# Kernel tuning notes

Hardware: AMD Instinct MI355X
Metric: run time of the kernel (lower is better)

The kernel has to match this reference:

```python
import jax, jax.numpy as jnp
import numpy as np

N_CHEM = 200000
N_GENE = 20000
N_EDGES = 1000000
IN, HID, OUT = 128, 256, 128


def _seg_mean(msg, dst, num_segments):
    # DGL fn.mean: mean of incoming messages; nodes with zero in-degree get 0.
    s = jax.ops.segment_sum(msg, dst, num_segments=num_segments)
    cnt = jax.ops.segment_sum(jnp.ones((msg.shape[0],), msg.dtype), dst,
                              num_segments=num_segments)[:, None]
    return jnp.where(cnt > 0, s / jnp.maximum(cnt, 1.0), 0.0)


def setup_inputs() -> dict:
    key = jax.random.key(0)
    ks = jax.random.split(key, 12)
    d = {
        'src_cg': jax.random.randint(ks[0], (N_EDGES,), 0, N_CHEM, dtype=jnp.int32),
        'dst_cg': jax.random.randint(ks[1], (N_EDGES,), 0, N_GENE, dtype=jnp.int32),
        'src_gc': jax.random.randint(ks[2], (N_EDGES,), 0, N_GENE, dtype=jnp.int32),
        'dst_gc': jax.random.randint(ks[3], (N_EDGES,), 0, N_CHEM, dtype=jnp.int32),
        'embed_chem': jax.random.normal(ks[4], (N_CHEM, IN), jnp.float32) * 0.1,
        'embed_gene': jax.random.normal(ks[5], (N_GENE, IN), jnp.float32) * 0.1,
        'W1_cg': jax.random.normal(ks[6], (IN, HID), jnp.float32) * (1.0 / np.sqrt(IN)),
        'b1_cg': jnp.zeros((HID,), jnp.float32),
        'W1_gc': jax.random.normal(ks[7], (IN, HID), jnp.float32) * (1.0 / np.sqrt(IN)),
        'b1_gc': jnp.zeros((HID,), jnp.float32),
        'W2_cg': jax.random.normal(ks[8], (HID, OUT), jnp.float32) * (1.0 / np.sqrt(HID)),
        'b2_cg': jnp.zeros((OUT,), jnp.float32),
        'W2_gc': jax.random.normal(ks[9], (HID, OUT), jnp.float32) * (1.0 / np.sqrt(HID)),
        'b2_gc': jnp.zeros((OUT,), jnp.float32),
    }
    return d


def _layer(h_chem, h_gene, W_cg, b_cg, W_gc, b_gc, src_cg, dst_cg, src_gc, dst_gc):
    # per-etype linear transform on source features
    Wh_cg = h_chem @ W_cg + b_cg   # [N_CHEM, D]
    Wh_gc = h_gene @ W_gc + b_gc   # [N_GENE, D]
    # copy_u + mean per etype; multi_update_all('sum') -> single etype per dst here
    new_gene = _seg_mean(Wh_cg[src_cg], dst_cg, N_GENE)
    new_chem = _seg_mean(Wh_gc[src_gc], dst_gc, N_CHEM)
    return new_chem, new_gene


def reference(src_cg, dst_cg, src_gc, dst_gc, embed_chem, embed_gene,
              W1_cg, b1_cg, W1_gc, b1_gc, W2_cg, b2_cg, W2_gc, b2_gc):
    h_chem, h_gene = _layer(embed_chem, embed_gene, W1_cg, b1_cg, W1_gc, b1_gc,
                            src_cg, dst_cg, src_gc, dst_gc)
    h_chem = jax.nn.leaky_relu(h_chem, negative_slope=0.01)
    h_gene = jax.nn.leaky_relu(h_gene, negative_slope=0.01)
    h_chem, _ = _layer(h_chem, h_gene, W2_cg, b2_cg, W2_gc, b2_gc,
                       src_cg, dst_cg, src_gc, dst_gc)
    return h_chem  # [N_CHEM, OUT]
```

## Files before the change

kernel.cpp:

```cpp
#include <hip/hip_runtime.h>
#include <stdint.h>
#include <stddef.h>

#define N_CHEM 200000
#define N_GENE 20000
#define N_EDGES 1000000
#define IN_D 128
#define HID_D 256
#define OUT_D 128
#define N_SEG (N_GENE + N_CHEM)

#define NGB 313
#define NCB 391
#define NB  (NGB + NCB)
#define EPB 2048
#define NBA ((2 * N_EDGES + EPB - 1) / EPB)
#define CAP 8192
#define DROPPED 0x80000000

typedef float nfloat4 __attribute__((ext_vector_type(4)));
typedef __attribute__((ext_vector_type(8))) short bf16x8;
typedef __attribute__((ext_vector_type(4))) float f32x4;

__device__ inline unsigned bf16rne(float x) {
    unsigned u = __float_as_uint(x);
    return (u + 0x7FFFu + ((u >> 16) & 1u)) >> 16;
}

__device__ inline int bucket_of(int slot) {
    return (slot < N_GENE) ? (slot >> 6) : (NGB + ((slot - N_GENE) >> 9));
}
__device__ inline int bucket_slot0(int b) {
    return (b < NGB) ? (b << 6) : (N_GENE + ((b - NGB) << 9));
}


__global__ __launch_bounds__(256) void place_convert_kernel(
        const int* __restrict__ src_cg, const int* __restrict__ dst_cg,
        const int* __restrict__ src_gc, const int* __restrict__ dst_gc,
        int* __restrict__ bcur, unsigned* __restrict__ records,
        const float* __restrict__ conv_in, unsigned short* __restrict__ conv_out) {
    if ((int)blockIdx.x >= NBA) {
        int cb = blockIdx.x - NBA;
        const int tid = threadIdx.x;
        #pragma unroll
        for (int q = 0; q < 4; ++q) {
            int i = cb * 1024 + q * 256 + tid;
            if (i < N_CHEM * IN_D / 4) {
                float4 v = *(const float4*)&conv_in[(size_t)i * 4];
                uint2 w;
                w.x = bf16rne(v.x) | (bf16rne(v.y) << 16);
                w.y = bf16rne(v.z) | (bf16rne(v.w) << 16);
                *(uint2*)&conv_out[(size_t)i * 4] = w;
            }
        }
        return;
    }
    __shared__ unsigned stage_rec[EPB];
    __shared__ unsigned short stage_bkt[EPB];
    __shared__ int hist[NB];
    __shared__ int cursor[NB];
    __shared__ int tsum[256];
    const int tid = threadIdx.x;
    const int e0 = blockIdx.x * EPB;
    const int cnt_blk = min(EPB, 2 * N_EDGES - e0);

    for (int i = tid; i < NB; i += 256) hist[i] = 0;
    __syncthreads();

    int slotR[EPB / 256], srcR[EPB / 256];
    #pragma unroll
    for (int q = 0; q < EPB / 256; ++q) {
        int e = e0 + q * 256 + tid;
        int slot = -1, s = 0;
        if (e < N_EDGES)            { slot = dst_cg[e];                    s = src_cg[e]; }
        else if (e < 2 * N_EDGES)   { slot = N_GENE + dst_gc[e - N_EDGES]; s = src_gc[e - N_EDGES]; }
        slotR[q] = slot; srcR[q] = s;
        if (slot >= 0) atomicAdd(&hist[bucket_of(slot)], 1);
    }
    __syncthreads();

    const int b3 = tid * 3;
    int h0 = (b3     < NB) ? hist[b3]     : 0;
    int h1 = (b3 + 1 < NB) ? hist[b3 + 1] : 0;
    int h2 = (b3 + 2 < NB) ? hist[b3 + 2] : 0;
    int ts = h0 + h1 + h2;
    tsum[tid] = ts;
    __syncthreads();
    for (int off = 1; off < 256; off <<= 1) {
        int t = (tid >= off) ? tsum[tid - off] : 0;
        __syncthreads();
        tsum[tid] += t;
        __syncthreads();
    }
    int base = tsum[tid] - ts;
    if (b3     < NB) cursor[b3]     = base;
    if (b3 + 1 < NB) cursor[b3 + 1] = base + h0;
    if (b3 + 2 < NB) cursor[b3 + 2] = base + h0 + h1;
    __syncthreads();

    #pragma unroll
    for (int q = 0; q < EPB / 256; ++q) {
        int slot = slotR[q];
        if (slot >= 0) {
            int b = bucket_of(slot);
            int p = atomicAdd(&cursor[b], 1);
            stage_rec[p] = ((unsigned)(slot - bucket_slot0(b)) << 18) | (unsigned)srcR[q];
            stage_bkt[p] = (unsigned short)b;
        }
    }
    __syncthreads();

    for (int i = tid; i < NB; i += 256) {
        int n = hist[i];
        if (n) {
            int got = atomicAdd(&bcur[i], n);
            int excl_i = cursor[i] - n;
            hist[i] = (got + n <= CAP) ? (i * CAP + got - excl_i) : (int)DROPPED;
        }
    }
    __syncthreads();

    for (int i = tid; i < cnt_blk; i += 256) {
        int d = hist[stage_bkt[i]];
        if (d != (int)DROPPED) records[i + d] = stage_rec[i];
    }
}


__global__ void bucket_scan_kernel(const int* __restrict__ bcur,
                                   int* __restrict__ bbase, int* __restrict__ indptr) {
    __shared__ int sm[1024];
    const int tid = threadIdx.x;
    int v = (tid < NB) ? min(bcur[tid], CAP) : 0;
    sm[tid] = v;
    __syncthreads();
    for (int off = 1; off < 1024; off <<= 1) {
        int t = (tid >= off) ? sm[tid - off] : 0;
        __syncthreads();
        sm[tid] += t;
        __syncthreads();
    }
    if (tid < NB) bbase[tid] = sm[tid] - v;
    if (tid == NB - 1) {
        bbase[NB] = sm[tid];
        indptr[N_SEG] = sm[tid];
    }
}


__global__ __launch_bounds__(256) void bin_b_kernel(
        const unsigned* __restrict__ records, const int* __restrict__ bbase,
        const int* __restrict__ bcur,
        int* __restrict__ indptr, int* __restrict__ esrc) {
    __shared__ int hist[512];
    __shared__ int tsum[256];
    const int tid = threadIdx.x;
    const int b = blockIdx.x;
    int slot0 = bucket_slot0(b);
    int nslots = (b < NGB) ? min(64, N_GENE - slot0) : min(512, N_SEG - slot0);
    const int rbase = bbase[b];
    const int E = min(bcur[b], CAP);
    const unsigned* rec = &records[(size_t)b * CAP];

    hist[tid] = 0; hist[tid + 256] = 0;
    __syncthreads();
    for (int i = tid; i < E; i += 256)
        atomicAdd(&hist[rec[i] >> 18], 1);
    __syncthreads();

    int h0 = hist[2 * tid], h1 = hist[2 * tid + 1];
    int ts = h0 + h1;
    tsum[tid] = ts;
    __syncthreads();
    for (int off = 1; off < 256; off <<= 1) {
        int t = (tid >= off) ? tsum[tid - off] : 0;
        __syncthreads();
        tsum[tid] += t;
        __syncthreads();
    }
    int ex = tsum[tid] - ts;
    __syncthreads();
    hist[2 * tid]     = ex;
    hist[2 * tid + 1] = ex + h0;
    if (2 * tid     < nslots) indptr[slot0 + 2 * tid]     = rbase + ex;
    if (2 * tid + 1 < nslots) indptr[slot0 + 2 * tid + 1] = rbase + ex + h0;
    __syncthreads();

    for (int i = tid; i < E; i += 256) {
        unsigned r = rec[i];
        int p = atomicAdd(&hist[r >> 18], 1);
        esrc[rbase + p] = (int)(r & 0x3FFFFu);
    }
}


__device__ inline void acc_u(float* a, uint4 v) {
    a[0] += __uint_as_float(v.x << 16); a[1] += __uint_as_float(v.x & 0xffff0000u);
    a[2] += __uint_as_float(v.y << 16); a[3] += __uint_as_float(v.y & 0xffff0000u);
    a[4] += __uint_as_float(v.z << 16); a[5] += __uint_as_float(v.z & 0xffff0000u);
    a[6] += __uint_as_float(v.w << 16); a[7] += __uint_as_float(v.w & 0xffff0000u);
}


__global__ __launch_bounds__(256) void gather_mean_bf16_split_kernel(
        const unsigned short* __restrict__ table,
        const int* __restrict__ indptr, const int* __restrict__ esrc,
        unsigned short* __restrict__ outb, int n) {
    int lane = threadIdx.x & 15;
    int half = (threadIdx.x >> 4) & 1;
    int node = blockIdx.x * 8 + (threadIdx.x >> 5);
    if (node >= n) return;
    int s = indptr[node], e = indptr[node + 1];
    int deg = e - s;
    int mid = s + ((deg + 1) >> 1);
    int j0 = half ? mid : s;
    int j1 = half ? e   : mid;
    int c = lane << 3;
    float acc[8] = {};
    int j = j0;
    for (; j + 8 <= j1; j += 8) {
        int i0 = esrc[j],     i1 = esrc[j + 1], i2 = esrc[j + 2], i3 = esrc[j + 3];
        int i4 = esrc[j + 4], i5 = esrc[j + 5], i6 = esrc[j + 6], i7 = esrc[j + 7];
        uint4 v0 = *(const uint4*)&table[(size_t)i0 * 128 + c];
        uint4 v1 = *(const uint4*)&table[(size_t)i1 * 128 + c];
        uint4 v2 = *(const uint4*)&table[(size_t)i2 * 128 + c];
        uint4 v3 = *(const uint4*)&table[(size_t)i3 * 128 + c];
        uint4 v4 = *(const uint4*)&table[(size_t)i4 * 128 + c];
        uint4 v5 = *(const uint4*)&table[(size_t)i5 * 128 + c];
        uint4 v6 = *(const uint4*)&table[(size_t)i6 * 128 + c];
        uint4 v7 = *(const uint4*)&table[(size_t)i7 * 128 + c];
        acc_u(acc, v0); acc_u(acc, v1); acc_u(acc, v2); acc_u(acc, v3);
        acc_u(acc, v4); acc_u(acc, v5); acc_u(acc, v6); acc_u(acc, v7);
    }
    for (; j + 4 <= j1; j += 4) {
        uint4 v0 = *(const uint4*)&table[(size_t)esrc[j]     * 128 + c];
        uint4 v1 = *(const uint4*)&table[(size_t)esrc[j + 1] * 128 + c];
        uint4 v2 = *(const uint4*)&table[(size_t)esrc[j + 2] * 128 + c];
        uint4 v3 = *(const uint4*)&table[(size_t)esrc[j + 3] * 128 + c];
        acc_u(acc, v0); acc_u(acc, v1); acc_u(acc, v2); acc_u(acc, v3);
    }
    for (; j < j1; ++j) {
        uint4 v = *(const uint4*)&table[(size_t)esrc[j] * 128 + c];
        acc_u(acc, v);
    }
    #pragma unroll
    for (int q = 0; q < 8; ++q) acc[q] += __shfl_xor(acc[q], 16);
    if (half == 0) {
        float inv = (deg > 0) ? 1.f / (float)deg : 0.f;
        #pragma unroll
        for (int q = 0; q < 8; ++q) acc[q] *= inv;
        uint4 w;
        w.x = bf16rne(acc[0]) | (bf16rne(acc[1]) << 16);
        w.y = bf16rne(acc[2]) | (bf16rne(acc[3]) << 16);
        w.z = bf16rne(acc[4]) | (bf16rne(acc[5]) << 16);
        w.w = bf16rne(acc[6]) | (bf16rne(acc[7]) << 16);
        *(uint4*)&outb[(size_t)node * 128 + c] = w;
    }
}


template<bool NT>
__global__ __launch_bounds__(256) void gather_mean_bf16_kernel(
        const unsigned short* __restrict__ table,
        const int* __restrict__ indptr, const int* __restrict__ esrc,
        float* __restrict__ out, int n) {
    int lane = threadIdx.x & 15;
    int node = blockIdx.x * 16 + (threadIdx.x >> 4);
    if (node >= n) return;
    int s = indptr[node], e = indptr[node + 1];
    int c = lane << 3;
    float acc[8] = {};
    int j = s;
    for (; j + 4 <= e; j += 4) {
        uint4 v0 = *(const uint4*)&table[(size_t)esrc[j]     * 128 + c];
        uint4 v1 = *(const uint4*)&table[(size_t)esrc[j + 1] * 128 + c];
        uint4 v2 = *(const uint4*)&table[(size_t)esrc[j + 2] * 128 + c];
        uint4 v3 = *(const uint4*)&table[(size_t)esrc[j + 3] * 128 + c];
        acc_u(acc, v0); acc_u(acc, v1); acc_u(acc, v2); acc_u(acc, v3);
    }
    for (; j < e; ++j) {
        uint4 v = *(const uint4*)&table[(size_t)esrc[j] * 128 + c];
        acc_u(acc, v);
    }
    int deg = e - s;
    float inv = (deg > 0) ? 1.f / (float)deg : 0.f;
    #pragma unroll
    for (int q = 0; q < 8; ++q) acc[q] *= inv;
    float* dst = &out[(size_t)node * 128 + c];
    if (NT) {
        nfloat4 a = { acc[0], acc[1], acc[2], acc[3] };
        nfloat4 b = { acc[4], acc[5], acc[6], acc[7] };
        __builtin_nontemporal_store(a, (nfloat4*)dst);
        __builtin_nontemporal_store(b, (nfloat4*)(dst + 4));
    } else {
        *(float4*)dst       = make_float4(acc[0], acc[1], acc[2], acc[3]);
        *(float4*)(dst + 4) = make_float4(acc[4], acc[5], acc[6], acc[7]);
    }
}


__global__ __launch_bounds__(256) void gather_mean_f32_kernel(
        const float* __restrict__ table,
        const int* __restrict__ indptr, const int* __restrict__ esrc,
        float* __restrict__ out, int n) {
    int lane = threadIdx.x & 31;
    int node = blockIdx.x * 8 + (threadIdx.x >> 5);
    if (node >= n) return;
    int s = indptr[node], e = indptr[node + 1];
    int c = lane << 2;
    float4 acc = make_float4(0.f, 0.f, 0.f, 0.f);
    int j = s;
    for (; j + 4 <= e; j += 4) {
        int s0 = esrc[j], s1 = esrc[j + 1], s2 = esrc[j + 2], s3 = esrc[j + 3];
        float4 v0 = *(const float4*)&table[(size_t)s0 * 128 + c];
        float4 v1 = *(const float4*)&table[(size_t)s1 * 128 + c];
        float4 v2 = *(const float4*)&table[(size_t)s2 * 128 + c];
        float4 v3 = *(const float4*)&table[(size_t)s3 * 128 + c];
        acc.x += (v0.x + v1.x) + (v2.x + v3.x);
        acc.y += (v0.y + v1.y) + (v2.y + v3.y);
        acc.z += (v0.z + v1.z) + (v2.z + v3.z);
        acc.w += (v0.w + v1.w) + (v2.w + v3.w);
    }
    for (; j < e; ++j) {
        float4 v = *(const float4*)&table[(size_t)esrc[j] * 128 + c];
        acc.x += v.x; acc.y += v.y; acc.z += v.z; acc.w += v.w;
    }
    int deg = e - s;
    float inv = (deg > 0) ? 1.f / (float)deg : 0.f;
    acc.x *= inv; acc.y *= inv; acc.z *= inv; acc.w *= inv;
    *(float4*)&out[(size_t)node * 128 + c] = acc;
}


template<int K, int N, bool MASK_LEAKY>
__global__ __launch_bounds__(256) void gemm_mfma_kernel(
        const unsigned short* __restrict__ A,
        const float* __restrict__ W,
        const float* __restrict__ bias,
        const int* __restrict__ indptr,
        unsigned short* __restrict__ C,
        int M) {
    constexpr int BK  = 128;
    constexpr int LDK = BK + 8;
    __shared__ unsigned short As[64 * LDK];
    __shared__ unsigned short Ws[64 * LDK];
    const int tid  = threadIdx.x;
    const int lane = tid & 63;
    const int w    = tid >> 6;
    const int m0 = blockIdx.x * 64;
    const int n0 = blockIdx.y * 64;
    const int l15 = lane & 15;
    const int lhi = lane >> 4;
    f32x4 acc[4] = {};

    for (int kt0 = 0; kt0 < K; kt0 += BK) {
        #pragma unroll
        for (int it = 0; it < 4; ++it) {
            int idx = it * 256 + tid;
            int row = idx >> 4;
            int c8  = (idx & 15) << 3;
            uint4 v = make_uint4(0u, 0u, 0u, 0u);
            if (m0 + row < M)
                v = *(const uint4*)&A[(size_t)(m0 + row) * K + kt0 + c8];
            *(uint4*)&As[row * LDK + c8] = v;
        }
        #pragma unroll
        for (int it = 0; it < 32; ++it) {
            int i = it * 256 + tid;
            int k = i >> 6;
            int n = i & 63;
            float f = W[(size_t)(kt0 + k) * N + n0 + n];
            Ws[n * LDK + k] = (unsigned short)bf16rne(f);
        }
        __syncthreads();

        #pragma unroll
        for (int kk = 0; kk < BK; kk += 32) {
            bf16x8 a = *(const bf16x8*)&As[(w * 16 + l15) * LDK + kk + lhi * 8];
            #pragma unroll
            for (int nt = 0; nt < 4; ++nt) {
                bf16x8 b = *(const bf16x8*)&Ws[(nt * 16 + l15) * LDK + kk + lhi * 8];
                acc[nt] = __builtin_amdgcn_mfma_f32_16x16x32_bf16(a, b, acc[nt], 0, 0, 0);
            }
        }
        __syncthreads();
    }

    #pragma unroll
    for (int nt = 0; nt < 4; ++nt) {
        int col = n0 + nt * 16 + l15;
        float bz = bias[col];
        #pragma unroll
        for (int r = 0; r < 4; ++r) {
            int row = m0 + w * 16 + lhi * 4 + r;
            if (row < M) {
                float v = acc[nt][r] + bz;
                if (MASK_LEAKY) {
                    int deg = indptr[row + 1] - indptr[row];
                    v = (deg == 0) ? 0.f : (v > 0.f ? v : 0.01f * v);
                }
                C[(size_t)row * N + col] = (unsigned short)bf16rne(v);
            }
        }
    }
}


template<int K, int N, bool MASK_LEAKY, bool BF16_OUT>
__global__ __launch_bounds__(256) void gemm_kernel(const float* __restrict__ A,
                                                   const float* __restrict__ W,
                                                   const float* __restrict__ bias,
                                                   const int* __restrict__ indptr,
                                                   void* __restrict__ Cout, int M) {
    __shared__ float As[64 * 68];
    __shared__ float Ws[64 * 64];
    const int tid = threadIdx.x;
    const int tx = tid & 15, ty = tid >> 4;
    const int m0 = blockIdx.x * 64;
    const int n0 = blockIdx.y * 64;
    const int r0 = ty << 2, c0 = tx << 2;
    float acc[4][4] = {};

    for (int kt = 0; kt < K; kt += 64) {
        #pragma unroll
        for (int q = 0; q < 4; ++q) {
            int idx = tid + q * 256;
            int row = idx >> 4;
            int c4  = (idx & 15) << 2;
            float4 v = make_float4(0.f, 0.f, 0.f, 0.f);
            if (m0 + row < M)
                v = *(const float4*)&A[(size_t)(m0 + row) * K + kt + c4];
            *(float4*)&As[row * 68 + c4] = v;
        }
        #pragma unroll
        for (int q = 0; q < 4; ++q) {
            int idx = tid + q * 256;
            int k   = idx >> 4;
            int c4  = (idx & 15) << 2;
            *(float4*)&Ws[(k << 6) + c4] =
                *(const float4*)&W[(size_t)(kt + k) * N + n0 + c4];
        }
        __syncthreads();

        #pragma unroll 4
        for (int k = 0; k < 64; k += 4) {
            float a[4][4];
            #pragma unroll
            for (int r = 0; r < 4; ++r) {
                float4 v = *(const float4*)&As[(r0 + r) * 68 + k];
                a[r][0] = v.x; a[r][1] = v.y; a[r][2] = v.z; a[r][3] = v.w;
            }
            #pragma unroll
            for (int kk = 0; kk < 4; ++kk) {
                float4 w = *(const float4*)&Ws[((k + kk) << 6) + c0];
                #pragma unroll
                for (int r = 0; r < 4; ++r) {
                    acc[r][0] = fmaf(a[r][kk], w.x, acc[r][0]);
                    acc[r][1] = fmaf(a[r][kk], w.y, acc[r][1]);
                    acc[r][2] = fmaf(a[r][kk], w.z, acc[r][2]);
                    acc[r][3] = fmaf(a[r][kk], w.w, acc[r][3]);
                }
            }
        }
        __syncthreads();
    }

    float4 b = *(const float4*)&bias[n0 + c0];
    #pragma unroll
    for (int r = 0; r < 4; ++r) {
        int row = m0 + r0 + r;
        if (row < M) {
            float4 v;
            v.x = acc[r][0] + b.x; v.y = acc[r][1] + b.y;
            v.z = acc[r][2] + b.z; v.w = acc[r][3] + b.w;
            if (MASK_LEAKY) {
                int deg = indptr[row + 1] - indptr[row];
                if (deg == 0) {
                    v = make_float4(0.f, 0.f, 0.f, 0.f);
                } else {
                    v.x = v.x > 0.f ? v.x : 0.01f * v.x;
                    v.y = v.y > 0.f ? v.y : 0.01f * v.y;
                    v.z = v.z > 0.f ? v.z : 0.01f * v.z;
                    v.w = v.w > 0.f ? v.w : 0.01f * v.w;
                }
            }
            if (BF16_OUT) {
                uint2 w;
                w.x = bf16rne(v.x) | (bf16rne(v.y) << 16);
                w.y = bf16rne(v.z) | (bf16rne(v.w) << 16);
                *(uint2*)&((unsigned short*)Cout)[(size_t)row * N + n0 + c0] = w;
            } else {
                *(float4*)&((float*)Cout)[(size_t)row * N + n0 + c0] = v;
            }
        }
    }
}


extern "C" void kernel_launch(void* const* d_in, const int* in_sizes, int n_in,
                              void* d_out, int out_size, void* d_ws, size_t ws_size,
                              hipStream_t stream) {
    const int*   src_cg     = (const int*)d_in[0];
    const int*   dst_cg     = (const int*)d_in[1];
    const int*   src_gc     = (const int*)d_in[2];
    const int*   dst_gc     = (const int*)d_in[3];
    const float* embed_chem = (const float*)d_in[4];
    const float* W1_cg = (const float*)d_in[6];
    const float* b1_cg = (const float*)d_in[7];
    const float* W2_gc = (const float*)d_in[12];
    const float* b2_gc = (const float*)d_in[13];
    float* out = (float*)d_out;

    int* ws_i = (int*)d_ws;
    size_t off = 0;
    int* bcur  = ws_i + off; off += NB;
    int* bbase = ws_i + off; off += NB + 1;
    off = (off + 3) & ~(size_t)3;
    int* indptr = ws_i + off; off += N_SEG + 1; off = (off + 3) & ~(size_t)3;
    int* esrc   = ws_i + off; off += 2 * N_EDGES;
    size_t union_off = off;
    unsigned* records = (unsigned*)(ws_i + union_off);
    unsigned short* agg1b   = (unsigned short*)(ws_i + union_off);
    unsigned short* h_geneb = agg1b + (size_t)N_GENE * IN_D;
    float* agg1f   = (float*)(ws_i + union_off);
    float* h_genef = agg1f + (size_t)N_GENE * IN_D;
    size_t union_sz = (size_t)N_GENE * (IN_D + HID_D);
    off = union_off + union_sz;
    unsigned short* Wh2b = (unsigned short*)(ws_i + off); off += (size_t)N_GENE * OUT_D / 2;
    unsigned short* embedb = (unsigned short*)(ws_i + off);
    size_t off_full = off + (size_t)N_CHEM * IN_D / 2;
    const bool bf16_embed = ws_size >= off_full * sizeof(int);

    (void)hipMemsetAsync(bcur, 0, NB * sizeof(int), stream);

    const int nconv = bf16_embed ? (N_CHEM * IN_D / 4 + 1023) / 1024 : 0;
    place_convert_kernel<<<NBA + nconv, 256, 0, stream>>>(
        src_cg, dst_cg, src_gc, dst_gc, bcur, records, embed_chem, embedb);
    bucket_scan_kernel<<<1, 1024, 0, stream>>>(bcur, bbase, indptr);
    bin_b_kernel<<<NB, 256, 0, stream>>>(records, bbase, bcur, indptr, esrc);

    if (bf16_embed) {
        gather_mean_bf16_split_kernel<<<(N_GENE + 7) / 8, 256, 0, stream>>>(
            embedb, indptr, esrc, agg1b, N_GENE);
        {
            dim3 g((N_GENE + 63) / 64, HID_D / 64), blk(256);
            gemm_mfma_kernel<IN_D, HID_D, true><<<g, blk, 0, stream>>>(
                agg1b, W1_cg, b1_cg, indptr, h_geneb, N_GENE);
        }
        {
            dim3 g((N_GENE + 63) / 64, OUT_D / 64), blk(256);
            gemm_mfma_kernel<HID_D, OUT_D, false><<<g, blk, 0, stream>>>(
                h_geneb, W2_gc, b2_gc, nullptr, Wh2b, N_GENE);
        }
    } else {
        gather_mean_f32_kernel<<<(N_GENE + 7) / 8, 256, 0, stream>>>(
            embed_chem, indptr, esrc, agg1f, N_GENE);
        {
            dim3 g((N_GENE + 63) / 64, HID_D / 64), blk(256);
            gemm_kernel<IN_D, HID_D, true, false><<<g, blk, 0, stream>>>(
                agg1f, W1_cg, b1_cg, indptr, h_genef, N_GENE);
        }
        {
            dim3 g((N_GENE + 63) / 64, OUT_D / 64), blk(256);
            gemm_kernel<HID_D, OUT_D, false, true><<<g, blk, 0, stream>>>(
                h_genef, W2_gc, b2_gc, nullptr, Wh2b, N_GENE);
        }
    }

    gather_mean_bf16_kernel<true><<<(N_CHEM + 15) / 16, 256, 0, stream>>>(
        Wh2b, indptr + N_GENE, esrc, out, N_CHEM);
}
```

Baseline: 387.6 us.

## Restructure gene and chem gather kernels and enlarge edges per placement block

The gene gather no longer splits each node's edge list between two half-warps. It now splits the feature columns into four 32-column slices spread across blocks, with four lanes per node, so each block's working set of the embedding table is narrower and more cache-friendly. The chem gather now uses 8 lanes per node, each loading 16 bf16 columns, and handles 32 nodes per block to raise bytes in flight per lane. The edge-placement blocking (EPB) doubles, halving the number of placement blocks. The risks are higher register use from 16 accumulators, fewer threads per node on the gene side, and possibly worse load balance in the placement phase.

New measurement: 484.1 us. 1.25x slower.

```diff
diff --git a/kernel.cpp b/kernel.cpp
--- a/kernel.cpp
+++ b/kernel.cpp
@@ -13,7 +13,7 @@
 #define NGB 313
 #define NCB 391
 #define NB  (NGB + NCB)
-#define EPB 2048
+#define EPB 4096
 #define NBA ((2 * N_EDGES + EPB - 1) / EPB)
 #define CAP 8192
 #define DROPPED 0x80000000
@@ -203,23 +203,20 @@
 }
 
 
-__global__ __launch_bounds__(256) void gather_mean_bf16_split_kernel(
+__global__ __launch_bounds__(256) void gather_gene_slice_kernel(
         const unsigned short* __restrict__ table,
         const int* __restrict__ indptr, const int* __restrict__ esrc,
         unsigned short* __restrict__ outb, int n) {
-    int lane = threadIdx.x & 15;
-    int half = (threadIdx.x >> 4) & 1;
-    int node = blockIdx.x * 8 + (threadIdx.x >> 5);
+    const int slice = blockIdx.x & 3;
+    const int g     = blockIdx.x >> 2;
+    const int lane  = threadIdx.x & 3;
+    const int node  = g * 64 + (threadIdx.x >> 2);
     if (node >= n) return;
     int s = indptr[node], e = indptr[node + 1];
-    int deg = e - s;
-    int mid = s + ((deg + 1) >> 1);
-    int j0 = half ? mid : s;
-    int j1 = half ? e   : mid;
-    int c = lane << 3;
+    int c = slice * 32 + lane * 8;
     float acc[8] = {};
-    int j = j0;
-    for (; j + 8 <= j1; j += 8) {
+    int j = s;
+    for (; j + 8 <= e; j += 8) {
         int i0 = esrc[j],     i1 = esrc[j + 1], i2 = esrc[j + 2], i3 = esrc[j + 3];
         int i4 = esrc[j + 4], i5 = esrc[j + 5], i6 = esrc[j + 6], i7 = esrc[j + 7];
         uint4 v0 = *(const uint4*)&table[(size_t)i0 * 128 + c];
@@ -233,52 +230,6 @@
         acc_u(acc, v0); acc_u(acc, v1); acc_u(acc, v2); acc_u(acc, v3);
         acc_u(acc, v4); acc_u(acc, v5); acc_u(acc, v6); acc_u(acc, v7);
     }
-    for (; j + 4 <= j1; j += 4) {
-        uint4 v0 = *(const uint4*)&table[(size_t)esrc[j]     * 128 + c];
-        uint4 v1 = *(const uint4*)&table[(size_t)esrc[j + 1] * 128 + c];
-        uint4 v2 = *(const uint4*)&table[(size_t)esrc[j + 2] * 128 + c];
-        uint4 v3 = *(const uint4*)&table[(size_t)esrc[j + 3] * 128 + c];
-        acc_u(acc, v0); acc_u(acc, v1); acc_u(acc, v2); acc_u(acc, v3);
-    }
-    for (; j < j1; ++j) {
-        uint4 v = *(const uint4*)&table[(size_t)esrc[j] * 128 + c];
-        acc_u(acc, v);
-    }
-    #pragma unroll
-    for (int q = 0; q < 8; ++q) acc[q] += __shfl_xor(acc[q], 16);
-    if (half == 0) {
-        float inv = (deg > 0) ? 1.f / (float)deg : 0.f;
-        #pragma unroll
-        for (int q = 0; q < 8; ++q) acc[q] *= inv;
-        uint4 w;
-        w.x = bf16rne(acc[0]) | (bf16rne(acc[1]) << 16);
-        w.y = bf16rne(acc[2]) | (bf16rne(acc[3]) << 16);
-        w.z = bf16rne(acc[4]) | (bf16rne(acc[5]) << 16);
-        w.w = bf16rne(acc[6]) | (bf16rne(acc[7]) << 16);
-        *(uint4*)&outb[(size_t)node * 128 + c] = w;
-    }
-}
-
-
-template<bool NT>
-__global__ __launch_bounds__(256) void gather_mean_bf16_kernel(
-        const unsigned short* __restrict__ table,
-        const int* __restrict__ indptr, const int* __restrict__ esrc,
-        float* __restrict__ out, int n) {
-    int lane = threadIdx.x & 15;
-    int node = blockIdx.x * 16 + (threadIdx.x >> 4);
-    if (node >= n) return;
-    int s = indptr[node], e = indptr[node + 1];
-    int c = lane << 3;
-    float acc[8] = {};
-    int j = s;
-    for (; j + 4 <= e; j += 4) {
-        uint4 v0 = *(const uint4*)&table[(size_t)esrc[j]     * 128 + c];
-        uint4 v1 = *(const uint4*)&table[(size_t)esrc[j + 1] * 128 + c];
-        uint4 v2 = *(const uint4*)&table[(size_t)esrc[j + 2] * 128 + c];
-        uint4 v3 = *(const uint4*)&table[(size_t)esrc[j + 3] * 128 + c];
-        acc_u(acc, v0); acc_u(acc, v1); acc_u(acc, v2); acc_u(acc, v3);
-    }
     for (; j < e; ++j) {
         uint4 v = *(const uint4*)&table[(size_t)esrc[j] * 128 + c];
         acc_u(acc, v);
@@ -287,16 +238,58 @@
     float inv = (deg > 0) ? 1.f / (float)deg : 0.f;
     #pragma unroll
     for (int q = 0; q < 8; ++q) acc[q] *= inv;
+    uint4 w;
+    w.x = bf16rne(acc[0]) | (bf16rne(acc[1]) << 16);
+    w.y = bf16rne(acc[2]) | (bf16rne(acc[3]) << 16);
+    w.z = bf16rne(acc[4]) | (bf16rne(acc[5]) << 16);
+    w.w = bf16rne(acc[6]) | (bf16rne(acc[7]) << 16);
+    *(uint4*)&outb[(size_t)node * 128 + c] = w;
+}
+
+
+__global__ __launch_bounds__(256) void gather_chem_kernel(
+        const unsigned short* __restrict__ table,
+        const int* __restrict__ indptr, const int* __restrict__ esrc,
+        float* __restrict__ out, int n) {
+    int lane = threadIdx.x & 7;
+    int node = blockIdx.x * 32 + (threadIdx.x >> 3);
+    if (node >= n) return;
+    int s = indptr[node], e = indptr[node + 1];
+    int c = lane << 4;
+    float acc[16] = {};
+    int j = s;
+    for (; j + 4 <= e; j += 4) {
+        const unsigned short* r0 = &table[(size_t)esrc[j]     * 128 + c];
+        const unsigned short* r1 = &table[(size_t)esrc[j + 1] * 128 + c];
+        const unsigned short* r2 = &table[(size_t)esrc[j + 2] * 128 + c];
+        const unsigned short* r3 = &table[(size_t)esrc[j + 3] * 128 + c];
+        uint4 a0 = *(const uint4*)r0, a1 = *(const uint4*)(r0 + 8);
+        uint4 b0 = *(const uint4*)r1, b1 = *(const uint4*)(r1 + 8);
+        uint4 c0 = *(const uint4*)r2, c1 = *(const uint4*)(r2 + 8);
+        uint4 d0 = *(const uint4*)r3, d1 = *(const uint4*)(r3 + 8);
+        acc_u(acc, a0); acc_u(acc + 8, a1);
+        acc_u(acc, b0); acc_u(acc + 8, b1);
+        acc_u(acc, c0); acc_u(acc + 8, c1);
+        acc_u(acc, d0); acc_u(acc + 8, d1);
+    }
+    for (; j < e; ++j) {
+        const unsigned short* r0 = &table[(size_t)esrc[j] * 128 + c];
+        uint4 a0 = *(const uint4*)r0, a1 = *(const uint4*)(r0 + 8);
+        acc_u(acc, a0); acc_u(acc + 8, a1);
+    }
+    int deg = e - s;
+    float inv = (deg > 0) ? 1.f / (float)deg : 0.f;
+    #pragma unroll
+    for (int q = 0; q < 16; ++q) acc[q] *= inv;
     float* dst = &out[(size_t)node * 128 + c];
-    if (NT) {
-        nfloat4 a = { acc[0], acc[1], acc[2], acc[3] };
-        nfloat4 b = { acc[4], acc[5], acc[6], acc[7] };
-        __builtin_nontemporal_store(a, (nfloat4*)dst);
-        __builtin_nontemporal_store(b, (nfloat4*)(dst + 4));
-    } else {
-        *(float4*)dst       = make_float4(acc[0], acc[1], acc[2], acc[3]);
-        *(float4*)(dst + 4) = make_float4(acc[4], acc[5], acc[6], acc[7]);
-    }
+    nfloat4 w0 = { acc[0],  acc[1],  acc[2],  acc[3]  };
+    nfloat4 w1 = { acc[4],  acc[5],  acc[6],  acc[7]  };
+    nfloat4 w2 = { acc[8],  acc[9],  acc[10], acc[11] };
+    nfloat4 w3 = { acc[12], acc[13], acc[14], acc[15] };
+    __builtin_nontemporal_store(w0, (nfloat4*)dst);
+    __builtin_nontemporal_store(w1, (nfloat4*)(dst + 4));
+    __builtin_nontemporal_store(w2, (nfloat4*)(dst + 8));
+    __builtin_nontemporal_store(w3, (nfloat4*)(dst + 12));
 }
 
 
@@ -541,7 +534,7 @@
     bin_b_kernel<<<NB, 256, 0, stream>>>(records, bbase, bcur, indptr, esrc);
 
     if (bf16_embed) {
-        gather_mean_bf16_split_kernel<<<(N_GENE + 7) / 8, 256, 0, stream>>>(
+        gather_gene_slice_kernel<<<4 * ((N_GENE + 63) / 64), 256, 0, stream>>>(
             embedb, indptr, esrc, agg1b, N_GENE);
         {
             dim3 g((N_GENE + 63) / 64, HID_D / 64), blk(256);
@@ -568,6 +561,6 @@
         }
     }
 
-    gather_mean_bf16_kernel<true><<<(N_CHEM + 15) / 16, 256, 0, stream>>>(
+    gather_chem_kernel<<<(N_CHEM + 31) / 32, 256, 0, stream>>>(
         Wh2b, indptr + N_GENE, esrc, out, N_CHEM);
 }
```
